# Kernel tuning notes

Measured on AMD Instinct MI355X. Metric: run time of the kernel, lower is better.

Reference implementation:

```python
import jax, jax.numpy as jnp
import numpy as np

B, S, D, H = 2, 2048, 4096, 32
HD = D // H  # 128
HALF = HD // 2  # 64


def setup_inputs() -> dict:
    key = jax.random.key(0)
    ks = jax.random.split(key, 6)
    scale = 1.0 / np.sqrt(D)
    x = jax.random.normal(ks[0], (B, S, D), jnp.float32)
    Wq = jax.random.normal(ks[1], (D, D), jnp.float32) * scale
    Wk = jax.random.normal(ks[2], (D, D), jnp.float32) * scale
    Wv = jax.random.normal(ks[3], (D, D), jnp.float32) * scale
    Wo = jax.random.normal(ks[4], (D, D), jnp.float32) * scale
    # Rotary frequencies: complex freqs of shape (S, HD//2) split into cos/sin
    inv_freq = 1.0 / (10000.0 ** (np.arange(0, HD, 2, dtype=np.float32) / HD))
    angles = np.outer(np.arange(S, dtype=np.float32), inv_freq)  # (S, HALF)
    freq_cos = jnp.asarray(np.cos(angles), jnp.float32)
    freq_sin = jnp.asarray(np.sin(angles), jnp.float32)
    # Additive causal mask (0 on/below diag, large-negative above)
    causal = jnp.tril(jnp.ones((S, S), jnp.bool_))
    mask = jnp.where(causal, 0.0, -1e9).astype(jnp.float32)
    return {"x": x, "Wq": Wq, "Wk": Wk, "Wv": Wv, "Wo": Wo,
            "freq_cos": freq_cos, "freq_sin": freq_sin, "mask": mask,
            "start_position": 0, "n_rep": 1}


def _apply_rope(t, freq_cos, freq_sin):
    # t: [B, S, H, HD]; complex multiply on interleaved (even, odd) pairs
    b, s, h, hd = t.shape
    tr = t.reshape(b, s, h, hd // 2, 2)
    a, c = tr[..., 0], tr[..., 1]
    cos = freq_cos[None, :, None, :]  # [1, S, 1, HALF]
    sin = freq_sin[None, :, None, :]
    out = jnp.stack([a * cos - c * sin, a * sin + c * cos], axis=-1)
    return out.reshape(b, s, h, hd)


def reference(x, Wq, Wk, Wv, Wo, freq_cos, freq_sin, mask, start_position, n_rep):
    b, s, _ = x.shape
    q = (x @ Wq).reshape(b, s, H, HD)
    k = (x @ Wk).reshape(b, s, H, HD)
    v = (x @ Wv).reshape(b, s, H, HD)
    q = _apply_rope(q, freq_cos, freq_sin)
    k = _apply_rope(k, freq_cos, freq_sin)
    if n_rep > 1:  # repeat_kv (identity when n_rep == 1)
        k = jnp.repeat(k, n_rep, axis=2)
        v = jnp.repeat(v, n_rep, axis=2)
    # KV-cache: with start_position=0 and s == max_sequence_length, the
    # cache slice [:, :start_position+s] equals the freshly written k/v.
    scores = jnp.einsum('bqhd,bkhd->bhqk', q, k) / jnp.sqrt(jnp.float32(HD))
    scores = scores + mask  # broadcast [S,S] over [B,H,S,S]
    weights = jax.nn.softmax(scores, axis=-1)
    out = jnp.einsum('bhqk,bkhd->bqhd', weights, v)
    out = out.reshape(b, s, H * HD)
    return out @ Wo
```

## Files before the change

### kernel.cpp

```cpp
#include <hip/hip_runtime.h>
#include <hip/hip_bf16.h>

#define DD 4096
#define MM 4096
#define SS 2048
#define HH 32
#define HDD 128
#define NT 64

typedef unsigned short u16;
typedef unsigned int u32;
typedef __attribute__((ext_vector_type(8))) __bf16 bf16x8;
typedef __attribute__((ext_vector_type(4))) float f32x4;
typedef __attribute__((ext_vector_type(4))) float float4v;
typedef __attribute__((ext_vector_type(8))) unsigned short ushort8;
typedef __attribute__((ext_vector_type(4))) unsigned int uint4v;

__device__ __forceinline__ u16 f2bf(float f) {
  union { float f; unsigned u; } v; v.f = f;
  unsigned u = v.u;
  return (u16)((u + 0x7fffu + ((u >> 16) & 1u)) >> 16);
}
__device__ __forceinline__ float bf2f(u16 s) {
  union { unsigned u; float f; } v; v.u = ((unsigned)s) << 16;
  return v.f;
}
__device__ __forceinline__ f32x4 zero4() { f32x4 z = {0.f, 0.f, 0.f, 0.f}; return z; }

__device__ __forceinline__ void gl_lds16(const u16* g, u16* l) {
  __builtin_amdgcn_global_load_lds((__attribute__((address_space(1))) void*)(g),
                                   (__attribute__((address_space(3))) void*)(l), 16, 0, 0);
}

__device__ __forceinline__ unsigned cvtpk(float lo, float hi) {
  unsigned r;
  asm("v_cvt_pk_bf16_f32 %0, %1, %2" : "=v"(r) : "v"(lo), "v"(hi));
  return r;
}
__device__ __forceinline__ u16 cvt1(float v) {
  unsigned r;
  asm("v_cvt_pk_bf16_f32 %0, %1, %1" : "=v"(r) : "v"(v));
  return (u16)r;
}
__device__ __forceinline__ float exp2a(float x) {
  float r;
  asm("v_exp_f32 %0, %1" : "=v"(r) : "v"(x));
  return r;
}

__global__ __launch_bounds__(256) void k_cvt(const float* __restrict__ in,
                                             u16* __restrict__ out, int n8) {
  int i = blockIdx.x * blockDim.x + threadIdx.x;
  if (i >= n8) return;
  size_t o = (size_t)i * 8;
  float4v a = *(const float4v*)(in + o);
  float4v b = *(const float4v*)(in + o + 4);
  ushort8 v;
  v[0] = f2bf(a[0]); v[1] = f2bf(a[1]); v[2] = f2bf(a[2]); v[3] = f2bf(a[3]);
  v[4] = f2bf(b[0]); v[5] = f2bf(b[1]); v[6] = f2bf(b[2]); v[7] = f2bf(b[3]);
  *(ushort8*)(out + o) = v;
}

__global__ __launch_bounds__(256) void k_wt(const float* __restrict__ W0,
                                            const float* __restrict__ W1,
                                            const float* __restrict__ W2,
                                            const float* __restrict__ W3,
                                            u16* __restrict__ out) {
  const float* W = blockIdx.z == 0 ? W0 : blockIdx.z == 1 ? W1 : blockIdx.z == 2 ? W2 : W3;
  u16* O = out + (size_t)blockIdx.z * DD * DD;
  __shared__ u16 t[64][66];
  int k0 = blockIdx.x * 64, n0 = blockIdx.y * 64;
  int tx = threadIdx.x, ty = threadIdx.y;
#pragma unroll
  for (int i = 0; i < 16; ++i) {
    int kk = ty + i * 4;
    t[tx][kk] = cvt1(W[(size_t)(k0 + kk) * DD + n0 + tx]);
  }
  __syncthreads();
  const int L = ty * 64 + tx;
  const int kx = L & 31, nb = L >> 5;
#pragma unroll
  for (int i = 0; i < 8; ++i) {
    int nn = nb + i * 8;
    u32 pk = *(const u32*)&t[nn][2 * kx];
    *(u32*)&O[(size_t)(n0 + nn) * DD + k0 + 2 * kx] = pk;
  }
}

#define MFMA16(QM, QN)                                                             \
  _Pragma("unroll") for (int kk = 0; kk < 2; ++kk)                                 \
  _Pragma("unroll") for (int mi = 0; mi < 4; ++mi)                                 \
  _Pragma("unroll") for (int ni = 0; ni < 2; ++ni)                                 \
      acc[(QM)*4 + mi][(QN)*2 + ni] = __builtin_amdgcn_mfma_f32_16x16x32_bf16(     \
          af[mi][kk], bf[(QN)*2 + ni][kk], acc[(QM)*4 + mi][(QN)*2 + ni], 0, 0, 0);

#define RDA2(P0, P1, QM)                                                           \
  _Pragma("unroll") for (int mi = 0; mi < 4; ++mi) {                               \
    af[mi][0] = *(const bf16x8*)((P0) + ((QM)*4 + mi) * 2048);                     \
    af[mi][1] = *(const bf16x8*)((P1) + ((QM)*4 + mi) * 2048);                     \
  }

#define RDB2(P0, P1, QN)                                                           \
  _Pragma("unroll") for (int ni = 0; ni < 2; ++ni) {                               \
    bf[(QN)*2 + ni][0] = *(const bf16x8*)((P0) + ((QN)*2 + ni) * 2048);            \
    bf[(QN)*2 + ni][1] = *(const bf16x8*)((P1) + ((QN)*2 + ni) * 2048);            \
  }

#define BAR() __builtin_amdgcn_s_barrier()
#define LGKM0() asm volatile("s_waitcnt lgkmcnt(0)" ::: "memory")
#define LGKM8() asm volatile("s_waitcnt lgkmcnt(8)" ::: "memory")
#define VM6() asm volatile("s_waitcnt vmcnt(6)" ::: "memory")
#define VM0() asm volatile("s_waitcnt vmcnt(0)" ::: "memory")
#define PRIO1() __builtin_amdgcn_s_setprio(1)
#define PRIO0() __builtin_amdgcn_s_setprio(0)

template <int MODE>
__global__ __launch_bounds__(512, 2) void k_gemm(const u16* __restrict__ A,
                                                 const u16* __restrict__ Bt,
                                                 void* __restrict__ Cout) {
  __shared__ __align__(16) u16 L[2][2][16384];
  const int tid = threadIdx.x;
  const int wid = tid >> 6, lane = tid & 63;
  const int g = lane >> 4, li = lane & 15;
  const int wr = wid >> 2, wc = wid & 3;

  const int bid = blockIdx.x;
  const int sw = ((bid & 7) << 5) | (bid >> 3);
  const int brow = (sw >> 4) * 256, bcol = (sw & 15) * 256;

  const int xsw = (li & 7) << 4;
  const int abase = (wr * 128 + li) * 128 + g * 16;
  const int bbase = (wc * 64 + li) * 128 + g * 16;

  const char* Lc = (const char*)&L[0][0][0];
  const char* aP00 = Lc + ((abase) ^ xsw);
  const char* aP01 = Lc + ((abase + 64) ^ xsw);
  const char* aP10 = Lc + 65536 + ((abase) ^ xsw);
  const char* aP11 = Lc + 65536 + ((abase + 64) ^ xsw);
  const char* bP00 = Lc + 32768 + ((bbase) ^ xsw);
  const char* bP01 = Lc + 32768 + ((bbase + 64) ^ xsw);
  const char* bP10 = Lc + 98304 + ((bbase) ^ xsw);
  const char* bP11 = Lc + 98304 + ((bbase + 64) ^ xsw);

  const int sxy = ((tid >> 3) & 7) << 3;
  const int scol = ((tid * 8) ^ sxy) & 63;
  const int srow0 = tid >> 3;
  const u16* gA0 = A + (size_t)(brow + srow0) * DD + scol;
  const u16* gA1 = A + (size_t)(brow + 128 + srow0) * DD + scol;
  const u16* gB0 = Bt + (size_t)(bcol + srow0) * DD + scol;
  const u16* gB1 = Bt + (size_t)(bcol + 128 + srow0) * DD + scol;
  u16* dA0b0 = &L[0][0][wid * 512];
  u16* dA1b0 = &L[0][0][8192 + wid * 512];
  u16* dB0b0 = &L[0][1][wid * 512];
  u16* dB1b0 = &L[0][1][8192 + wid * 512];
  u16* dA0b1 = &L[1][0][wid * 512];
  u16* dA1b1 = &L[1][0][8192 + wid * 512];
  u16* dB0b1 = &L[1][1][wid * 512];
  u16* dB1b1 = &L[1][1][8192 + wid * 512];

  auto SH = [&](const u16* gsrc, u16* ld) {
    gl_lds16(gsrc, ld);
    gl_lds16(gsrc + (size_t)64 * DD, ld + 4096);
  };

  f32x4 acc[8][4];
#pragma unroll
  for (int m = 0; m < 8; ++m)
#pragma unroll
    for (int n = 0; n < 4; ++n) acc[m][n] = zero4();

  bf16x8 af[4][2], bf[4][2];

  SH(gA0, dA0b0); SH(gA1, dA1b0); SH(gB0, dB0b0); SH(gB1, dB1b0);
  SH(gA0 + 64, dA0b1); SH(gB0 + 64, dB0b1); SH(gB1 + 64, dB1b1);
  VM6();
  BAR();

  for (int it = 0; it < 31; ++it) {
    const u16* a0 = gA0 + it * 128;
    const u16* a1 = gA1 + it * 128;
    const u16* b0 = gB0 + it * 128;
    const u16* b1 = gB1 + it * 128;
    RDA2(aP00, aP01, 0); RDB2(bP00, bP01, 0);
    SH(a1 + 64, dA1b1);
    LGKM8();
    BAR(); LGKM0();
    PRIO1(); MFMA16(0, 0); PRIO0();
    BAR();
    RDB2(bP00, bP01, 1);
    BAR(); LGKM0();
    PRIO1(); MFMA16(0, 1); PRIO0();
    BAR();
    RDA2(aP00, aP01, 1);
    SH(b0 + 128, dB0b0);
    BAR(); LGKM0();
    PRIO1(); MFMA16(1, 0); PRIO0();
    BAR();
    SH(b1 + 128, dB1b0);
    SH(a0 + 128, dA0b0);
    VM6();
    BAR(); LGKM0();
    PRIO1(); MFMA16(1, 1); PRIO0();
    BAR();
    RDA2(aP10, aP11, 0); RDB2(bP10, bP11, 0);
    SH(a1 + 128, dA1b0);
    LGKM8();
    BAR(); LGKM0();
    PRIO1(); MFMA16(0, 0); PRIO0();
    BAR();
    RDB2(bP10, bP11, 1);
    BAR(); LGKM0();
    PRIO1(); MFMA16(0, 1); PRIO0();
    BAR();
    RDA2(aP10, aP11, 1);
    SH(b0 + 192, dB0b1);
    BAR(); LGKM0();
    PRIO1(); MFMA16(1, 0); PRIO0();
    BAR();
    SH(b1 + 192, dB1b1);
    SH(a0 + 192, dA0b1);
    VM6();
    BAR(); LGKM0();
    PRIO1(); MFMA16(1, 1); PRIO0();
    BAR();
  }

  {
    const u16* a1 = gA1 + 31 * 128;
    RDA2(aP00, aP01, 0); RDB2(bP00, bP01, 0);
    SH(a1 + 64, dA1b1);
    LGKM8();
    BAR(); LGKM0();
    PRIO1(); MFMA16(0, 0); PRIO0();
    BAR();
    RDB2(bP00, bP01, 1);
    BAR(); LGKM0();
    PRIO1(); MFMA16(0, 1); PRIO0();
    BAR();
    RDA2(aP00, aP01, 1);
    BAR(); LGKM0();
    PRIO1(); MFMA16(1, 0); PRIO0();
    BAR();
    VM0();
    BAR(); LGKM0();
    PRIO1(); MFMA16(1, 1); PRIO0();
    BAR();
  }
  {
    RDA2(aP10, aP11, 0); RDB2(bP10, bP11, 0);
    BAR(); LGKM0();
    PRIO1(); MFMA16(0, 0); PRIO0();
    BAR();
    RDB2(bP10, bP11, 1);
    BAR(); LGKM0();
    PRIO1(); MFMA16(0, 1); PRIO0();
    BAR();
    RDA2(aP10, aP11, 1);
    BAR(); LGKM0();
    PRIO1(); MFMA16(1, 0); PRIO0();
    BAR();
    BAR(); LGKM0();
    PRIO1(); MFMA16(1, 1); PRIO0();
    BAR();
  }

#pragma unroll
  for (int m = 0; m < 8; ++m) {
#pragma unroll
    for (int n = 0; n < 4; ++n) {
#pragma unroll
      for (int r = 0; r < 4; ++r) {
        int row = brow + wr * 128 + m * 16 + g * 4 + r;
        int col = bcol + wc * 64 + n * 16 + li;
        float v = acc[m][n][r];
        if (MODE == 0) {
          ((u16*)Cout)[(size_t)row * DD + col] = cvt1(v);
        } else if (MODE == 1) {
          ((u16*)Cout)[((size_t)((row >> 11) << 12) + col) * SS + (row & 2047)] = cvt1(v);
        } else {
          ((float*)Cout)[(size_t)row * DD + col] = v;
        }
      }
    }
  }
}

__global__ __launch_bounds__(256) void k_rope(u16* __restrict__ Q, u16* __restrict__ Kp,
                                              const float* __restrict__ fc,
                                              const float* __restrict__ fs) {
  int idx = blockIdx.x * blockDim.x + threadIdx.x;
  const int n8 = MM * DD / 8;
  const float qsc = idx < n8 ? 0.08838834764831845f * 1.44269504088896340f : 1.0f;
  u16* T = idx < n8 ? Q : Kp;
  int i = idx < n8 ? idx : idx - n8;
  int m = i >> 9;
  int c = (i & 511) * 8;
  int s = m & (SS - 1);
  int i0 = (c & (HDD - 1)) >> 1;
  size_t o = (size_t)m * DD + c;
  ushort8 v = *(ushort8*)(T + o);
  float4v cs = *(const float4v*)(fc + s * 64 + i0);
  float4v sn = *(const float4v*)(fs + s * 64 + i0);
  ushort8 ov;
#pragma unroll
  for (int p = 0; p < 4; ++p) {
    float a = bf2f(v[2 * p]), cc = bf2f(v[2 * p + 1]);
    ov[2 * p]     = cvt1((a * cs[p] - cc * sn[p]) * qsc);
    ov[2 * p + 1] = cvt1((a * sn[p] + cc * cs[p]) * qsc);
  }
  *(ushort8*)(T + o) = ov;
}

__global__ __launch_bounds__(256) void k_attn(const u16* __restrict__ Q,
                                              const u16* __restrict__ K,
                                              const u16* __restrict__ VT,
                                              u16* __restrict__ O) {
  __shared__ __align__(16) u16 Kl[2][32 * 128];
  __shared__ __align__(16) u16 Vl[2][128 * 32];
  __shared__ __align__(16) u16 Pl[4][16 * 32];
  const int bh = blockIdx.x;
  const int qt = 31 - blockIdx.y;
  const int b = bh >> 5, h = bh & 31;
  const int tid = threadIdx.x, w = tid >> 6, lane = tid & 63;
  const int g = lane >> 4, li = lane & 15;

  const u16* Qbase = Q + ((size_t)(b * SS + qt * 64 + w * 16 + li)) * DD + h * HDD;
  const u16* Kbase = K + ((size_t)(b * SS)) * DD + h * HDD;
  const u16* Vbase = VT + ((size_t)bh) * HDD * SS;

  bf16x8 qf[4];
#pragma unroll
  for (int ks = 0; ks < 4; ++ks)
    qf[ks] = *(const bf16x8*)(Qbase + ks * 32 + g * 8);

  f32x4 oa[8];
#pragma unroll
  for (int f = 0; f < 8; ++f) oa[f] = zero4();
  float lrun = 0.f;
  const int wli = w * 16 + li;

  const int krow0 = w * 8 + (lane >> 4);
  const int ksg0 = (lane & 15) ^ (lane >> 4);
  const int ksg1 = (lane & 15) ^ (4 + (lane >> 4));
  const int vdr0 = w * 16 + (lane >> 2);
  const int va0 = (vdr0 * 64 + (lane & 3) * 16) ^ (((vdr0 >> 1) & 7) << 4);
  const int vdr1 = vdr0 + 64;
  const int va1 = (vdr1 * 64 + (lane & 3) * 16) ^ (((vdr1 >> 1) & 7) << 4);

  auto STAGE = [&](int t, int nb) {
    const u16* Kt = Kbase + (size_t)(t * 32) * DD;
    gl_lds16(Kt + (size_t)krow0 * DD + ksg0 * 8, &Kl[nb][(w * 8) * 128]);
    gl_lds16(Kt + (size_t)(krow0 + 4) * DD + ksg1 * 8, &Kl[nb][(w * 8 + 4) * 128]);
    const u16* Vt = Vbase + t * 32;
    gl_lds16(Vt + (size_t)(va0 >> 6) * SS + ((va0 >> 4) & 3) * 8, &Vl[nb][w * 512]);
    gl_lds16(Vt + (size_t)(va1 >> 6) * SS + ((va1 >> 4) & 3) * 8, &Vl[nb][2048 + w * 512]);
  };

  auto TILE = [&](int kt, int cb, int koff) __attribute__((always_inline)) {
    f32x4 sc[2];
    sc[0] = zero4(); sc[1] = zero4();
    PRIO1();
#pragma unroll
    for (int ks = 0; ks < 4; ++ks) {
#pragma unroll
      for (int ktg = 0; ktg < 2; ++ktg) {
        int kr = ktg * 16 + li;
        int off = (kr * 256 + (ks * 32 + g * 8) * 2) ^ ((kr & 7) << 4);
        bf16x8 kf = *(const bf16x8*)((const char*)Kl[cb] + off);
        sc[ktg] = __builtin_amdgcn_mfma_f32_16x16x32_bf16(kf, qf[ks], sc[ktg], 0, 0, 0);
      }
    }
    PRIO0();

    float p[8];
    float su = 0.f;
#pragma unroll
    for (int ktg = 0; ktg < 2; ++ktg) {
#pragma unroll
      for (int r = 0; r < 4; ++r) {
        float s = sc[ktg][r];
        if (koff >= 0 && (koff + ktg * 16 + g * 4 + r > wli)) s = -1e30f;
        float pv = exp2a(s - 16.f);
        p[ktg * 4 + r] = pv;
        su += pv;
      }
    }
    su += __shfl_xor(su, 16);
    su += __shfl_xor(su, 32);
    lrun += su;

    {
      char* Pb = (char*)Pl[w];
      const int swz = ((li >> 1) & 7) << 4;
#pragma unroll
      for (int ktg = 0; ktg < 2; ++ktg) {
#pragma unroll
        for (int j = 0; j < 2; ++j) {
          unsigned pk = cvtpk(p[ktg * 4 + 2 * j], p[ktg * 4 + 2 * j + 1]);
          int off = (li * 64 + ktg * 32 + g * 8 + 4 * j) ^ swz;
          *(unsigned*)(Pb + off) = pk;
        }
      }
    }
    asm volatile("s_waitcnt lgkmcnt(0)" ::: "memory");

    PRIO1();
    {
      int poff = (li * 64 + g * 16) ^ (((li >> 1) & 7) << 4);
      bf16x8 pfrag = *(const bf16x8*)((const char*)Pl[w] + poff);
#pragma unroll
      for (int f = 0; f < 8; ++f) {
        int dr = f * 16 + li;
        int voff = (dr * 64 + g * 16) ^ (((dr >> 1) & 7) << 4);
        bf16x8 vf = *(const bf16x8*)((const char*)Vl[cb] + voff);
        oa[f] = __builtin_amdgcn_mfma_f32_16x16x32_bf16(pfrag, vf, oa[f], 0, 0, 0);
      }
    }
    PRIO0();

    asm volatile("s_waitcnt vmcnt(0)" ::: "memory");
    __syncthreads();
  };

  STAGE(0, 0);
  asm volatile("s_waitcnt vmcnt(0)" ::: "memory");
  __syncthreads();

  for (int i = 0; i < qt; ++i) {
    STAGE(2 * i + 1, 1);
    TILE(2 * i, 0, -1);
    STAGE(2 * i + 2, 0);
    TILE(2 * i + 1, 1, -1);
  }
  STAGE(2 * qt + 1, 1);
  TILE(2 * qt, 0, 0);
  TILE(2 * qt + 1, 1, 32);

  float lv[4];
#pragma unroll
  for (int r = 0; r < 4; ++r) lv[r] = __shfl(lrun, g * 20 + r);
  u16* Ob = O + ((size_t)(b * SS + qt * 64 + w * 16 + g * 4)) * DD + h * HDD;
#pragma unroll
  for (int r = 0; r < 4; ++r) {
    float inv = 1.f / lv[r];
#pragma unroll
    for (int f = 0; f < 8; ++f)
      Ob[(size_t)r * DD + f * 16 + li] = cvt1(oa[f][r] * inv);
  }
}

extern "C" void kernel_launch(void* const* d_in, const int* in_sizes, int n_in,
                              void* d_out, int out_size, void* d_ws, size_t ws_size,
                              hipStream_t stream) {
  (void)in_sizes; (void)n_in; (void)out_size; (void)ws_size;
  const float* x    = (const float*)d_in[0];
  const float* Wq   = (const float*)d_in[1];
  const float* Wk   = (const float*)d_in[2];
  const float* Wv   = (const float*)d_in[3];
  const float* Wo   = (const float*)d_in[4];
  const float* fcos = (const float*)d_in[5];
  const float* fsin = (const float*)d_in[6];

  u16* ws = (u16*)d_ws;
  const size_t MAT = (size_t)4096 * 4096;
  u16* xb    = ws + 0 * MAT;
  u16* wqt   = ws + 1 * MAT;
  u16* wkt   = ws + 2 * MAT;
  u16* wvt   = ws + 3 * MAT;
  u16* wot   = ws + 4 * MAT;
  u16* Qb    = ws + 5 * MAT;
  u16* Kb    = ws + 6 * MAT;
  u16* VTb   = ws + 7 * MAT;
  u16* attnb = ws + 8 * MAT;

  k_cvt<<<dim3(8192), dim3(256), 0, stream>>>(x, xb, (int)(MAT / 8));
  k_wt<<<dim3(64, 64, 4), dim3(64, 4), 0, stream>>>(Wq, Wk, Wv, Wo, wqt);
  k_gemm<0><<<dim3(256), dim3(512), 0, stream>>>(xb, wqt, (void*)Qb);
  k_gemm<0><<<dim3(256), dim3(512), 0, stream>>>(xb, wkt, (void*)Kb);
  k_gemm<1><<<dim3(256), dim3(512), 0, stream>>>(xb, wvt, (void*)VTb);
  k_rope<<<dim3(16384), dim3(256), 0, stream>>>(Qb, Kb, fcos, fsin);
  k_attn<<<dim3(64, 32), dim3(256), 0, stream>>>(Qb, Kb, VTb, attnb);
  k_gemm<2><<<dim3(256), dim3(512), 0, stream>>>(attnb, wot, d_out);
}
```

Measured before the change: 742.8 us.

## Add 128x256-tile GEMM variant with higher occupancy and use it for K projection

Adds a new GEMM kernel that uses 128x256 output tiles with a 32-wide K step, double-buffered direct global-to-LDS loads, and a swizzled LDS layout. It launches 512 blocks with launch bounds allowing four blocks per CU instead of two. Only the K projection switches to it; the Q, V and output GEMMs keep the old kernel. The smaller tile raises occupancy and block count but lowers data reuse per block and adds more barriers per K step.

```diff
diff --git a/kernel.cpp b/kernel.cpp
--- a/kernel.cpp
+++ b/kernel.cpp
@@ -87,6 +87,15 @@
   }
 }
 
+#define BAR() __builtin_amdgcn_s_barrier()
+#define LGKM0() asm volatile("s_waitcnt lgkmcnt(0)" ::: "memory")
+#define LGKM8() asm volatile("s_waitcnt lgkmcnt(8)" ::: "memory")
+#define VM6() asm volatile("s_waitcnt vmcnt(6)" ::: "memory")
+#define VM3() asm volatile("s_waitcnt vmcnt(3)" ::: "memory")
+#define VM0() asm volatile("s_waitcnt vmcnt(0)" ::: "memory")
+#define PRIO1() __builtin_amdgcn_s_setprio(1)
+#define PRIO0() __builtin_amdgcn_s_setprio(0)
+
 #define MFMA16(QM, QN)                                                             \
   _Pragma("unroll") for (int kk = 0; kk < 2; ++kk)                                 \
   _Pragma("unroll") for (int mi = 0; mi < 4; ++mi)                                 \
@@ -105,14 +114,6 @@
     bf[(QN)*2 + ni][0] = *(const bf16x8*)((P0) + ((QN)*2 + ni) * 2048);            \
     bf[(QN)*2 + ni][1] = *(const bf16x8*)((P1) + ((QN)*2 + ni) * 2048);            \
   }
-
-#define BAR() __builtin_amdgcn_s_barrier()
-#define LGKM0() asm volatile("s_waitcnt lgkmcnt(0)" ::: "memory")
-#define LGKM8() asm volatile("s_waitcnt lgkmcnt(8)" ::: "memory")
-#define VM6() asm volatile("s_waitcnt vmcnt(6)" ::: "memory")
-#define VM0() asm volatile("s_waitcnt vmcnt(0)" ::: "memory")
-#define PRIO1() __builtin_amdgcn_s_setprio(1)
-#define PRIO0() __builtin_amdgcn_s_setprio(0)
 
 template <int MODE>
 __global__ __launch_bounds__(512, 2) void k_gemm(const u16* __restrict__ A,
@@ -271,6 +272,104 @@
 #pragma unroll
       for (int r = 0; r < 4; ++r) {
         int row = brow + wr * 128 + m * 16 + g * 4 + r;
+        int col = bcol + wc * 64 + n * 16 + li;
+        float v = acc[m][n][r];
+        if (MODE == 0) {
+          ((u16*)Cout)[(size_t)row * DD + col] = cvt1(v);
+        } else if (MODE == 1) {
+          ((u16*)Cout)[((size_t)((row >> 11) << 12) + col) * SS + (row & 2047)] = cvt1(v);
+        } else {
+          ((float*)Cout)[(size_t)row * DD + col] = v;
+        }
+      }
+    }
+  }
+}
+
+#define GTILE2(AP, BP, T, STG, WAIT)                                               \
+  {                                                                                \
+    _Pragma("unroll") for (int mi = 0; mi < 4; ++mi)                               \
+        af[mi] = *(const bf16x8*)((AP) + mi * 1024);                               \
+    _Pragma("unroll") for (int ni = 0; ni < 4; ++ni)                               \
+        bfr[ni] = *(const bf16x8*)((BP) + ni * 1024);                              \
+    LGKM0();                                                                       \
+    BAR();                                                                         \
+    if (STG) {                                                                     \
+      const int k0 = (T + 2) << 5;                                                 \
+      gl_lds16(gA + k0, dA[(T)&1]);                                                \
+      gl_lds16(gB0 + k0, dB0[(T)&1]);                                              \
+      gl_lds16(gB1 + k0, dB1[(T)&1]);                                              \
+    }                                                                              \
+    WAIT();                                                                        \
+    PRIO1();                                                                       \
+    _Pragma("unroll") for (int mi = 0; mi < 4; ++mi)                               \
+    _Pragma("unroll") for (int ni = 0; ni < 4; ++ni)                               \
+        acc[mi][ni] =                                                              \
+            __builtin_amdgcn_mfma_f32_16x16x32_bf16(af[mi], bfr[ni], acc[mi][ni], 0, 0, 0); \
+    PRIO0();                                                                       \
+    BAR();                                                                         \
+  }
+
+template <int MODE>
+__global__ __launch_bounds__(512, 4) void k_gemm2(const u16* __restrict__ A,
+                                                  const u16* __restrict__ Bt,
+                                                  void* __restrict__ Cout) {
+  __shared__ __align__(16) u16 LA[2][4096];
+  __shared__ __align__(16) u16 LB[2][8192];
+  const int tid = threadIdx.x;
+  const int wid = tid >> 6, lane = tid & 63;
+  const int g = lane >> 4, li = lane & 15;
+  const int wr = wid >> 2, wc = wid & 3;
+
+  const int bid = blockIdx.x;
+  const int sw = ((bid & 7) << 6) | (bid >> 3);
+  const int brow = (sw >> 4) * 128, bcol = (sw & 15) * 256;
+
+  const int gs = (g ^ ((li >> 1) & 3)) * 16;
+  const char* LAc = (const char*)&LA[0][0];
+  const char* LBc = (const char*)&LB[0][0];
+  const int aoff = (wr * 64 + li) * 64 + gs;
+  const int boff = (wc * 64 + li) * 64 + gs;
+  const char* aP[2] = {LAc + aoff, LAc + 8192 + aoff};
+  const char* bP[2] = {LBc + boff, LBc + 16384 + boff};
+
+  const int srow = tid >> 2;
+  const int scol = ((tid & 3) ^ ((tid >> 3) & 3)) * 8;
+  const u16* gA = A + (size_t)(brow + srow) * DD + scol;
+  const u16* gB0 = Bt + (size_t)(bcol + srow) * DD + scol;
+  const u16* gB1 = Bt + (size_t)(bcol + 128 + srow) * DD + scol;
+  u16* dA[2] = {&LA[0][wid * 512], &LA[1][wid * 512]};
+  u16* dB0[2] = {&LB[0][wid * 512], &LB[1][wid * 512]};
+  u16* dB1[2] = {&LB[0][4096 + wid * 512], &LB[1][4096 + wid * 512]};
+
+  f32x4 acc[4][4];
+#pragma unroll
+  for (int m = 0; m < 4; ++m)
+#pragma unroll
+    for (int n = 0; n < 4; ++n) acc[m][n] = zero4();
+
+  bf16x8 af[4], bfr[4];
+
+  gl_lds16(gA, dA[0]); gl_lds16(gB0, dB0[0]); gl_lds16(gB1, dB1[0]);
+  gl_lds16(gA + 32, dA[1]); gl_lds16(gB0 + 32, dB0[1]); gl_lds16(gB1 + 32, dB1[1]);
+  VM3();
+  BAR();
+
+  for (int it = 0; it < 63; ++it) {
+    const int t0 = 2 * it;
+    GTILE2(aP[0], bP[0], t0, 1, VM3);
+    GTILE2(aP[1], bP[1], t0 + 1, 1, VM3);
+  }
+  GTILE2(aP[0], bP[0], 126, 0, VM0);
+  GTILE2(aP[1], bP[1], 127, 0, VM0);
+
+#pragma unroll
+  for (int m = 0; m < 4; ++m) {
+#pragma unroll
+    for (int n = 0; n < 4; ++n) {
+#pragma unroll
+      for (int r = 0; r < 4; ++r) {
+        int row = brow + wr * 64 + m * 16 + g * 4 + r;
         int col = bcol + wc * 64 + n * 16 + li;
         float v = acc[m][n][r];
         if (MODE == 0) {
@@ -476,7 +575,7 @@
   k_cvt<<<dim3(8192), dim3(256), 0, stream>>>(x, xb, (int)(MAT / 8));
   k_wt<<<dim3(64, 64, 4), dim3(64, 4), 0, stream>>>(Wq, Wk, Wv, Wo, wqt);
   k_gemm<0><<<dim3(256), dim3(512), 0, stream>>>(xb, wqt, (void*)Qb);
-  k_gemm<0><<<dim3(256), dim3(512), 0, stream>>>(xb, wkt, (void*)Kb);
+  k_gemm2<0><<<dim3(512), dim3(512), 0, stream>>>(xb, wkt, (void*)Kb);
   k_gemm<1><<<dim3(256), dim3(512), 0, stream>>>(xb, wvt, (void*)VTb);
   k_rope<<<dim3(16384), dim3(256), 0, stream>>>(Qb, Kb, fcos, fsin);
   k_attn<<<dim3(64, 32), dim3(256), 0, stream>>>(Qb, Kb, VTb, attnb);
```

Measured after the change: 762.0 us. 2.6% more time.
